# Kernel tuning notes

Measured on AMD Instinct MI355X. Metric: run time of the kernel, lower is better.

The kernel has to match this reference:

```python
import jax, jax.numpy as jnp
import numpy as np

HUMAN_EXHALATION_FLOW = 0.0052  # ENV_CONFIG.HUMAN_EXHALATION_FLOW
TIME_STEP = 1.0                 # ENV_CONFIG.TIME_STEP
N_NODES = 100_000
N_EDGES = 3_200_000
IN_DIM, OUT_DIM, K = 4, 1, 3
T_HIST = 16


def setup_inputs() -> dict:
    key = jax.random.key(0)
    k1, k2, k3, k4, k5 = jax.random.split(key, 5)
    # columns at [:, -1, :]: 0=concentration, 1=people, 2=size (size divides -> keep away from 0)
    origin_data = jax.random.uniform(k1, (N_NODES, T_HIST, 3), jnp.float32, 0.5, 1.5)
    # raw flow field: conv with kernel K (VALID) maps [E+K-1, K, IN_DIM] -> [E, 1, OUT_DIM]
    flow = jax.random.normal(k2, (N_EDGES + K - 1, K, IN_DIM), jnp.float32)
    edge_index = jax.random.randint(k3, (2, N_EDGES), 0, N_NODES, jnp.int32)
    conv_w = jax.random.normal(k4, (OUT_DIM, IN_DIM, K, K), jnp.float32) * 0.1
    conv_b = jax.random.normal(k5, (OUT_DIM,), jnp.float32) * 0.1
    return {"origin_data": origin_data, "flow": flow, "conv_w": conv_w,
            "conv_b": conv_b, "edge_index": edge_index}


def _flow_conv(flow, conv_w, conv_b):
    # [H, W, C] -> [1, C, H, W] -> conv -> [H', W', out_dim]
    x = jnp.transpose(flow, (2, 0, 1))[None]
    y = jax.lax.conv_general_dilated(
        x, conv_w, window_strides=(1, 1), padding='VALID',
        dimension_numbers=('NCHW', 'OIHW', 'NCHW'))
    y = y + conv_b[None, :, None, None]
    return jnp.transpose(y[0], (1, 2, 0))  # [E, 1, out_dim]


def reference(origin_data, flow, conv_w, conv_b, edge_index):
    concentration = origin_data[:, -1, 0]  # [N]
    people = origin_data[:, -1, 1]         # [N]
    size = origin_data[:, -1, 2]           # [N]
    n = concentration.shape[0]
    mask = jnp.ones((n,), concentration.dtype).at[-1].set(0.0)

    fc = _flow_conv(flow, conv_w, conv_b)  # [E, 1, 1]
    val = fc[:, 0, 0]                      # [E]

    src, dst = edge_index[0], edge_index[1]
    # original loop uses .item() everywhere -> these terms are detached from autodiff
    c_sg = jax.lax.stop_gradient(concentration)
    s_sg = jax.lax.stop_gradient(size)
    v_sg = jax.lax.stop_gradient(val)
    msg = jnp.where(src != dst, v_sg * c_sg[src], 0.0)  # skip self-loops
    node_new = jnp.zeros((n,), concentration.dtype)
    node_new = node_new.at[src].add(-msg / s_sg[src] * TIME_STEP)
    node_new = node_new.at[dst].add(msg / s_sg[dst] * TIME_STEP)

    exhaled = HUMAN_EXHALATION_FLOW * jax.lax.stop_gradient(people) / s_sg  # .item() loop -> detached
    result = concentration + (node_new + exhaled * TIME_STEP) * mask
    out2 = jnp.concatenate([edge_index.T.astype(val.dtype), fc[:, :, 0]], axis=1)  # [E, 3]
    return result[:, None], out2
```

## Files before the change

### kernel.cpp

```cpp
#include <hip/hip_runtime.h>


#define WSH  13
#define WSZ  8192
#define SL   20
#define EPT  4
#define MAXW 32

#define OWSH 13
#define OWSZ 8192
#define OPB  16
#define OFPS 8192.0f
#define OQBIAS (1 << 20)
#define OQCLMP ((1 << 19) - 1)

__global__ __launch_bounds__(256) void prep(
    const float* __restrict__ od,
    float* __restrict__ conc,
    unsigned long long* __restrict__ acc,
    unsigned* __restrict__ tails,
    int n_nodes)
{
    if (blockIdx.x == 0 && tails && threadIdx.x < 65)
        tails[(size_t)threadIdx.x << 4] = 0u;
    int n = blockIdx.x * blockDim.x + threadIdx.x;
    if (n >= n_nodes) return;
    conc[n] = od[(long long)n * 48 + 45];
    if (acc) acc[n] = 0ULL;
}

__global__ __launch_bounds__(256) void edge_scatter(
    const float* __restrict__ flow, const int* __restrict__ ei,
    const float* __restrict__ conv_w, const float* __restrict__ conv_b,
    const float* __restrict__ conc,
    float* __restrict__ out2,
    uint2* __restrict__ recA, uint2* __restrict__ recB,
    uint2* __restrict__ ovf,
    unsigned* __restrict__ tails,
    int n_edges, unsigned cap, unsigned ocap)
{
    __shared__ float w[40];
    __shared__ unsigned cnt[2 * MAXW];
    __shared__ unsigned bas[2 * MAXW];
    const int t = threadIdx.x;
    if (t < 36) {
        int i  = t & 3;
        int kw = (t >> 2) % 3;
        int kh = t / 12;
        w[t] = conv_w[i * 9 + kh * 3 + kw];
    }
    if (t == 36) w[36] = conv_b[0];
    if (t < 2 * MAXW) cnt[t] = 0u;
    __syncthreads();

    const long long eb = (long long)blockIdx.x * (256 * EPT) + t;
    int      sN[EPT], dN[EPT];
    float    vA[EPT], vB[EPT];
    unsigned pA_[EPT], pB_[EPT];
    bool     live[EPT];

#pragma unroll
    for (int k = 0; k < EPT; ++k) {
        long long e = eb + (long long)k * 256;
        live[k] = false;
        if (e < n_edges) {
            int s = ei[e];
            int d = ei[n_edges + e];
            const float4* fp = (const float4*)(flow + e * 12);
            float acc = w[36];
#pragma unroll
            for (int q = 0; q < 9; ++q) {
                float4 v = fp[q];
                acc = fmaf(v.x, w[q * 4 + 0], acc);
                acc = fmaf(v.y, w[q * 4 + 1], acc);
                acc = fmaf(v.z, w[q * 4 + 2], acc);
                acc = fmaf(v.w, w[q * 4 + 3], acc);
            }
            float cs = conc[s];
            float* o = out2 + e * 3;
            o[0] = (float)s;
            o[1] = (float)d;
            o[2] = acc;
            sN[k] = s; dN[k] = d;
            vA[k] = acc; vB[k] = acc * cs;
            if (s != d) {
                live[k] = true;
                pA_[k] = atomicAdd(&cnt[(unsigned)s >> WSH], 1u);
                pB_[k] = atomicAdd(&cnt[MAXW + ((unsigned)d >> WSH)], 1u);
            }
        }
    }
    __syncthreads();
    if (t < 2 * MAXW && cnt[t])
        bas[t] = atomicAdd(&tails[(size_t)t << 4], cnt[t]);
    __syncthreads();

#pragma unroll
    for (int k = 0; k < EPT; ++k) {
        if (!live[k]) continue;
        {
            unsigned wa = (unsigned)sN[k] >> WSH;
            unsigned sa = bas[wa] + pA_[k];
            uint2 r; r.x = (unsigned)sN[k]; r.y = __float_as_uint(vA[k]);
            if (sa < cap) {
                recA[(size_t)wa * cap + sa] = r;
            } else {
                unsigned os = atomicAdd(&tails[(size_t)64 << 4], 1u);
                if (os < ocap) ovf[os] = r;
            }
        }
        {
            unsigned wb = (unsigned)dN[k] >> WSH;
            unsigned sb = bas[MAXW + wb] + pB_[k];
            uint2 r; r.x = (unsigned)dN[k]; r.y = __float_as_uint(vB[k]);
            if (sb < cap) {
                recB[(size_t)wb * cap + sb] = r;
            } else {
                r.x |= 0x80000000u;
                unsigned os = atomicAdd(&tails[(size_t)64 << 4], 1u);
                if (os < ocap) ovf[os] = r;
            }
        }
    }
}

__global__ __launch_bounds__(1024) void accum_b(
    const uint2* __restrict__ recA, const uint2* __restrict__ recB,
    const uint2* __restrict__ ovf,
    const unsigned* __restrict__ tails,
    float* __restrict__ pA, float* __restrict__ pB,
    unsigned cap, unsigned ocap)
{
    __shared__ float tA[WSZ];
    __shared__ float tB[WSZ];

    const int w  = blockIdx.x / SL;
    const int sl = blockIdx.x % SL;
    const int t  = threadIdx.x;

    for (int i = t; i < WSZ; i += 1024) { tA[i] = 0.f; tB[i] = 0.f; }
    __syncthreads();

    {
        unsigned nA = min(tails[(size_t)w << 4], cap);
        const uint2* r = recA + (size_t)w * cap;
        size_t i0 = (size_t)nA * sl / SL, i1 = (size_t)nA * (sl + 1) / SL;
        for (size_t i = i0 + t; i < i1; i += 1024) {
            uint2 q = r[i];
            atomicAdd(&tA[q.x & (WSZ - 1)], __uint_as_float(q.y));
        }
    }
    {
        unsigned nB = min(tails[(size_t)(MAXW + w) << 4], cap);
        const uint2* r = recB + (size_t)w * cap;
        size_t i0 = (size_t)nB * sl / SL, i1 = (size_t)nB * (sl + 1) / SL;
        for (size_t i = i0 + t; i < i1; i += 1024) {
            uint2 q = r[i];
            atomicAdd(&tB[q.x & (WSZ - 1)], __uint_as_float(q.y));
        }
    }
    {
        unsigned no = min(tails[(size_t)64 << 4], ocap);
        if (no) {
            size_t i0 = (size_t)no * sl / SL, i1 = (size_t)no * (sl + 1) / SL;
            for (size_t i = i0 + t; i < i1; i += 1024) {
                uint2 q = ovf[i];
                unsigned node = q.x & 0x7fffffffu;
                if ((int)(node >> WSH) == w) {
                    if (q.x >> 31) atomicAdd(&tB[node & (WSZ - 1)], __uint_as_float(q.y));
                    else           atomicAdd(&tA[node & (WSZ - 1)], __uint_as_float(q.y));
                }
            }
        }
    }
    __syncthreads();

    float* dA = pA + ((size_t)blockIdx.x << WSH);
    float* dB = pB + ((size_t)blockIdx.x << WSH);
    for (int i = t; i < (WSZ >> 2); i += 1024) {
        ((float4*)dA)[i] = ((const float4*)tA)[i];
        ((float4*)dB)[i] = ((const float4*)tB)[i];
    }
}

__global__ __launch_bounds__(256) void node_final_b(
    const float* __restrict__ od,
    const float* __restrict__ conc,
    const float* __restrict__ pA,
    const float* __restrict__ pB,
    float* __restrict__ out, int n_nodes)
{
    int n = blockIdx.x * blockDim.x + threadIdx.x;
    if (n >= n_nodes) return;

    const int w = n >> WSH, i = n & (WSZ - 1);
    size_t base = ((size_t)(w * SL) << WSH) + i;
    float a = 0.f, b = 0.f;
#pragma unroll
    for (int sl = 0; sl < SL; ++sl) {
        a += pA[base + ((size_t)sl << WSH)];
        b += pB[base + ((size_t)sl << WSH)];
    }

    long long bi = (long long)n * 48 + 45;
    float c  = conc[n];
    float p  = od[bi + 1];
    float is = 1.0f / od[bi + 2];

    float r = c;
    if (n != n_nodes - 1)
        r += (b - a * c) * is + 0.0052f * p * is;
    out[n] = r;
}

__global__ __launch_bounds__(256) void edge_conv_o(
    const float* __restrict__ flow, const int* __restrict__ ei,
    const float* __restrict__ conv_w, const float* __restrict__ conv_b,
    float* __restrict__ out2, int n_edges)
{
    __shared__ float w[40];
    int t = threadIdx.x;
    if (t < 36) {
        int i  = t & 3;
        int kw = (t >> 2) % 3;
        int kh = t / 12;
        w[t] = conv_w[i * 9 + kh * 3 + kw];
    }
    if (t == 36) w[36] = conv_b[0];
    __syncthreads();

    int e = blockIdx.x * blockDim.x + t;
    if (e >= n_edges) return;

    const float4* fp = (const float4*)(flow + (long long)e * 12);
    float acc = w[36];
#pragma unroll
    for (int q = 0; q < 9; ++q) {
        float4 v = fp[q];
        acc = fmaf(v.x, w[q * 4 + 0], acc);
        acc = fmaf(v.y, w[q * 4 + 1], acc);
        acc = fmaf(v.z, w[q * 4 + 2], acc);
        acc = fmaf(v.w, w[q * 4 + 3], acc);
    }

    float* o = out2 + (long long)e * 3;
    o[0] = (float)ei[e];
    o[1] = (float)ei[n_edges + e];
    o[2] = acc;
}

__global__ __launch_bounds__(1024) void accum_o(
    const float* __restrict__ out2,
    const float* __restrict__ conc,
    unsigned long long* __restrict__ acc,
    int n_edges, int n_nodes)
{
    __shared__ float tA[OWSZ];
    __shared__ float tB[OWSZ];

    const int w    = blockIdx.x / OPB;
    const int sl   = blockIdx.x % OPB;
    const int base = w << OWSH;

    for (int i = threadIdx.x; i < OWSZ; i += 1024) { tA[i] = 0.f; tB[i] = 0.f; }
    __syncthreads();

    const long long e0 = (long long)sl * n_edges / OPB;
    const long long e1 = (long long)(sl + 1) * n_edges / OPB;
    for (long long e = e0 + threadIdx.x; e < e1; e += 1024) {
        const float* r = out2 + e * 3;
        float fs = r[0], fd = r[1], v = r[2];
        int s = (int)fs, d = (int)fd;
        if (s == d) continue;
        if ((s >> OWSH) == w) atomicAdd(&tA[s - base], v);
        if ((d >> OWSH) == w) atomicAdd(&tB[d - base], v * conc[s]);
    }
    __syncthreads();

    for (int i = threadIdx.x; i < OWSZ; i += 1024) {
        int n = base + i;
        if (n >= n_nodes) continue;
        float a = tA[i], b = tB[i];
        if (a == 0.f && b == 0.f) continue;
        int qa = __float2int_rn(a * OFPS);
        int qb = __float2int_rn(b * OFPS);
        qa = min(max(qa, -OQCLMP), OQCLMP);
        qb = min(max(qb, -OQCLMP), OQCLMP);
        unsigned long long enc =
            ((unsigned long long)(unsigned)(qa + OQBIAS) << 37) +
            ((unsigned long long)(unsigned)(qb + OQBIAS) << 10) + 1ULL;
        atomicAdd(acc + n, enc);
    }
}

__global__ __launch_bounds__(256) void node_final_o(
    const float* __restrict__ od,
    const float* __restrict__ conc,
    const unsigned long long* __restrict__ acc,
    float* __restrict__ out, int n_nodes)
{
    int n = blockIdx.x * blockDim.x + threadIdx.x;
    if (n >= n_nodes) return;

    unsigned long long t = acc[n];
    long long cnt = (long long)(t & 1023ULL);
    unsigned long long t2 = t >> 10;
    long long sbr = (long long)(t2 & ((1ULL << 27) - 1));
    long long sar = (long long)(t2 >> 27);
    float a = (float)(sar - cnt * OQBIAS) * (1.0f / OFPS);
    float b = (float)(sbr - cnt * OQBIAS) * (1.0f / OFPS);

    long long bi = (long long)n * 48 + 45;
    float c  = conc[n];
    float p  = od[bi + 1];
    float is = 1.0f / od[bi + 2];

    float r = c;
    if (n != n_nodes - 1)
        r += (b - a * c) * is + 0.0052f * p * is;
    out[n] = r;
}

extern "C" void kernel_launch(void* const* d_in, const int* in_sizes, int n_in,
                              void* d_out, int out_size, void* d_ws, size_t ws_size,
                              hipStream_t stream) {
    const float* od   = (const float*)d_in[0];
    const float* flow = (const float*)d_in[1];
    const float* cw   = (const float*)d_in[2];
    const float* cb   = (const float*)d_in[3];
    const int*   ei   = (const int*)d_in[4];

    const int n_nodes = in_sizes[0] / 48;
    const int n_edges = in_sizes[4] / 2;

    float* out_res = (float*)d_out;
    float* out2    = out_res + n_nodes;

    dim3 blk(256);
    dim3 grid_nodes((n_nodes + 255) / 256);

    const int n_win = (n_nodes + WSZ - 1) >> WSH;
    const unsigned cap  = (unsigned)(n_edges / (n_win > 0 ? n_win : 1))
                        + (unsigned)(n_edges / 8) + 1024u;
    const unsigned ocap = (unsigned)(2ULL * (unsigned long long)n_edges);

    size_t off = 0;
    size_t o_conc  = off; off += (((size_t)n_nodes * 4) + 255) & ~255ULL;
    size_t o_tails = off; off += (65 * 16 * 4 + 255) & ~255ULL;
    size_t o_recA  = off; off += (((size_t)n_win * cap * 8) + 255) & ~255ULL;
    size_t o_recB  = off; off += (((size_t)n_win * cap * 8) + 255) & ~255ULL;
    size_t o_ovf   = off; off += (((size_t)ocap * 8) + 255) & ~255ULL;
    size_t o_pA    = off; off += (((size_t)n_win * SL * WSZ * 4) + 255) & ~255ULL;
    size_t o_pB    = off; off += (((size_t)n_win * SL * WSZ * 4) + 255) & ~255ULL;
    const bool full = (ws_size >= off) && (n_win <= MAXW);

    float* conc = (float*)((char*)d_ws + o_conc);

    if (full) {
        unsigned* tails = (unsigned*)((char*)d_ws + o_tails);
        uint2* recA = (uint2*)((char*)d_ws + o_recA);
        uint2* recB = (uint2*)((char*)d_ws + o_recB);
        uint2* ovf  = (uint2*)((char*)d_ws + o_ovf);
        float* pA   = (float*)((char*)d_ws + o_pA);
        float* pB   = (float*)((char*)d_ws + o_pB);

        dim3 grid_es((n_edges + 256 * EPT - 1) / (256 * EPT));

        prep<<<grid_nodes, blk, 0, stream>>>(od, conc, nullptr, tails, n_nodes);
        edge_scatter<<<grid_es, blk, 0, stream>>>(flow, ei, cw, cb, conc,
                                                  out2, recA, recB, ovf, tails,
                                                  n_edges, cap, ocap);
        accum_b<<<dim3(n_win * SL), dim3(1024), 0, stream>>>(
            recA, recB, ovf, tails, pA, pB, cap, ocap);
        node_final_b<<<grid_nodes, blk, 0, stream>>>(od, conc, pA, pB,
                                                     out_res, n_nodes);
    } else {
        unsigned long long* acc =
            (unsigned long long*)((char*)d_ws + (((size_t)n_nodes * 4 + 7) / 8 * 8));
        const int n_win_o = (n_nodes + OWSZ - 1) >> OWSH;
        dim3 grid_edges((n_edges + 255) / 256);

        prep<<<grid_nodes, blk, 0, stream>>>(od, conc, acc, nullptr, n_nodes);
        edge_conv_o<<<grid_edges, blk, 0, stream>>>(flow, ei, cw, cb, out2, n_edges);
        accum_o<<<dim3(n_win_o * OPB), dim3(1024), 0, stream>>>(
            out2, conc, acc, n_edges, n_nodes);
        node_final_o<<<grid_nodes, blk, 0, stream>>>(od, conc, acc,
                                                     out_res, n_nodes);
    }
}
```

Measured before the change: 341.4 us.

## Stage scatter records in LDS, coalesce writes, and use wider node windows

The edge scatter kernel now sorts each block's records by bucket in shared memory and writes them out contiguously, so the global record stores are coalesced instead of scattered. Window size doubles to 16K nodes with 32 slices per window, which reduces the number of buckets and changes the accumulation grid. The recA/recB buffers merge into one bucketed array, and the partial-sum reduction is split into two accumulators. The cost is extra LDS use (about 24KB per block) and an added barrier in edge_scatter, plus larger per-block shared tables in accum_b, which may lower occupancy.

Measured after the change: 344.1 us. Within noise of the previous version (+0.8%).

```diff
diff --git a/kernel.cpp b/kernel.cpp
--- a/kernel.cpp
+++ b/kernel.cpp
@@ -1,11 +1,12 @@
 #include <hip/hip_runtime.h>
 
 
-#define WSH  13
-#define WSZ  8192
-#define SL   20
-#define EPT  4
-#define MAXW 32
+#define WSH    14
+#define WSZ    16384
+#define SLC    32
+#define EPT    4
+#define MAXWIN 16
+#define OVSLOT 32
 
 #define OWSH 13
 #define OWSZ 8192
@@ -21,7 +22,7 @@
     unsigned* __restrict__ tails,
     int n_nodes)
 {
-    if (blockIdx.x == 0 && tails && threadIdx.x < 65)
+    if (blockIdx.x == 0 && tails && threadIdx.x <= OVSLOT)
         tails[(size_t)threadIdx.x << 4] = 0u;
     int n = blockIdx.x * blockDim.x + threadIdx.x;
     if (n >= n_nodes) return;
@@ -34,15 +35,21 @@
     const float* __restrict__ conv_w, const float* __restrict__ conv_b,
     const float* __restrict__ conc,
     float* __restrict__ out2,
-    uint2* __restrict__ recA, uint2* __restrict__ recB,
+    uint2* __restrict__ rec,
     uint2* __restrict__ ovf,
     unsigned* __restrict__ tails,
-    int n_edges, unsigned cap, unsigned ocap)
-{
-    __shared__ float w[40];
-    __shared__ unsigned cnt[2 * MAXW];
-    __shared__ unsigned bas[2 * MAXW];
-    const int t = threadIdx.x;
+    int n_edges, int n_win, unsigned cap, unsigned ocap)
+{
+    __shared__ float    w[40];
+    __shared__ unsigned cnt[2 * MAXWIN];
+    __shared__ unsigned sst[2 * MAXWIN];
+    __shared__ unsigned bas[2 * MAXWIN];
+    __shared__ unsigned stot;
+    __shared__ uint2    stg[512 * EPT];
+    __shared__ unsigned dsti[512 * EPT];
+
+    const int t  = threadIdx.x;
+    const int NB = 2 * n_win;
     if (t < 36) {
         int i  = t & 3;
         int kw = (t >> 2) % 3;
@@ -50,19 +57,17 @@
         w[t] = conv_w[i * 9 + kh * 3 + kw];
     }
     if (t == 36) w[36] = conv_b[0];
-    if (t < 2 * MAXW) cnt[t] = 0u;
+    if (t < 2 * MAXWIN) cnt[t] = 0u;
     __syncthreads();
 
     const long long eb = (long long)blockIdx.x * (256 * EPT) + t;
-    int      sN[EPT], dN[EPT];
-    float    vA[EPT], vB[EPT];
-    unsigned pA_[EPT], pB_[EPT];
-    bool     live[EPT];
+    uint2    payA[EPT], payB[EPT];
+    unsigned posA[EPT], posB[EPT];
 
 #pragma unroll
     for (int k = 0; k < EPT; ++k) {
+        posA[k] = 0xffffffffu; posB[k] = 0xffffffffu;
         long long e = eb + (long long)k * 256;
-        live[k] = false;
         if (e < n_edges) {
             int s = ei[e];
             int d = ei[n_edges + e];
@@ -81,89 +86,107 @@
             o[0] = (float)s;
             o[1] = (float)d;
             o[2] = acc;
-            sN[k] = s; dN[k] = d;
-            vA[k] = acc; vB[k] = acc * cs;
             if (s != d) {
-                live[k] = true;
-                pA_[k] = atomicAdd(&cnt[(unsigned)s >> WSH], 1u);
-                pB_[k] = atomicAdd(&cnt[MAXW + ((unsigned)d >> WSH)], 1u);
+                payA[k].x = (unsigned)s; payA[k].y = __float_as_uint(acc);
+                payB[k].x = (unsigned)d; payB[k].y = __float_as_uint(acc * cs);
+                posA[k] = atomicAdd(&cnt[(unsigned)s >> WSH], 1u);
+                posB[k] = atomicAdd(&cnt[n_win + ((unsigned)d >> WSH)], 1u);
             }
         }
     }
     __syncthreads();
-    if (t < 2 * MAXW && cnt[t])
-        bas[t] = atomicAdd(&tails[(size_t)t << 4], cnt[t]);
+
+    if (t == 0) {
+        unsigned a = 0;
+        for (int b = 0; b < NB; ++b) { sst[b] = a; a += cnt[b]; }
+        stot = a;
+    }
+    if (t < NB && cnt[t]) bas[t] = atomicAdd(&tails[(size_t)t << 4], cnt[t]);
     __syncthreads();
 
 #pragma unroll
     for (int k = 0; k < EPT; ++k) {
-        if (!live[k]) continue;
-        {
-            unsigned wa = (unsigned)sN[k] >> WSH;
-            unsigned sa = bas[wa] + pA_[k];
-            uint2 r; r.x = (unsigned)sN[k]; r.y = __float_as_uint(vA[k]);
-            if (sa < cap) {
-                recA[(size_t)wa * cap + sa] = r;
+        if (posA[k] != 0xffffffffu) {
+            unsigned b = payA[k].x >> WSH;
+            unsigned i = sst[b] + posA[k];
+            unsigned g = bas[b] + posA[k];
+            stg[i] = payA[k];
+            if (g < cap) {
+                dsti[i] = b * cap + g;
             } else {
-                unsigned os = atomicAdd(&tails[(size_t)64 << 4], 1u);
-                if (os < ocap) ovf[os] = r;
+                dsti[i] = 0xffffffffu;
+                unsigned os = atomicAdd(&tails[(size_t)OVSLOT << 4], 1u);
+                if (os < ocap) ovf[os] = payA[k];
             }
         }
-        {
-            unsigned wb = (unsigned)dN[k] >> WSH;
-            unsigned sb = bas[MAXW + wb] + pB_[k];
-            uint2 r; r.x = (unsigned)dN[k]; r.y = __float_as_uint(vB[k]);
-            if (sb < cap) {
-                recB[(size_t)wb * cap + sb] = r;
+        if (posB[k] != 0xffffffffu) {
+            unsigned b = n_win + (payB[k].x >> WSH);
+            unsigned i = sst[b] + posB[k];
+            unsigned g = bas[b] + posB[k];
+            stg[i] = payB[k];
+            if (g < cap) {
+                dsti[i] = b * cap + g;
             } else {
-                r.x |= 0x80000000u;
-                unsigned os = atomicAdd(&tails[(size_t)64 << 4], 1u);
-                if (os < ocap) ovf[os] = r;
+                dsti[i] = 0xffffffffu;
+                unsigned os = atomicAdd(&tails[(size_t)OVSLOT << 4], 1u);
+                if (os < ocap) { uint2 r = payB[k]; r.x |= 0x80000000u; ovf[os] = r; }
             }
         }
     }
+    __syncthreads();
+
+    unsigned tot = stot;
+    for (unsigned i = t; i < tot; i += 256) {
+        unsigned u = dsti[i];
+        if (u != 0xffffffffu) rec[u] = stg[i];
+    }
 }
 
 __global__ __launch_bounds__(1024) void accum_b(
-    const uint2* __restrict__ recA, const uint2* __restrict__ recB,
-    const uint2* __restrict__ ovf,
+    const uint2* __restrict__ rec, const uint2* __restrict__ ovf,
     const unsigned* __restrict__ tails,
     float* __restrict__ pA, float* __restrict__ pB,
-    unsigned cap, unsigned ocap)
+    int n_win, unsigned cap, unsigned ocap)
 {
     __shared__ float tA[WSZ];
     __shared__ float tB[WSZ];
 
-    const int w  = blockIdx.x / SL;
-    const int sl = blockIdx.x % SL;
+    const int w  = blockIdx.x / SLC;
+    const int sl = blockIdx.x % SLC;
     const int t  = threadIdx.x;
 
-    for (int i = t; i < WSZ; i += 1024) { tA[i] = 0.f; tB[i] = 0.f; }
+    float4 z = make_float4(0.f, 0.f, 0.f, 0.f);
+    for (int i = t; i < (WSZ >> 2); i += 1024) {
+        ((float4*)tA)[i] = z; ((float4*)tB)[i] = z;
+    }
     __syncthreads();
 
     {
         unsigned nA = min(tails[(size_t)w << 4], cap);
-        const uint2* r = recA + (size_t)w * cap;
-        size_t i0 = (size_t)nA * sl / SL, i1 = (size_t)nA * (sl + 1) / SL;
-        for (size_t i = i0 + t; i < i1; i += 1024) {
+        const uint2* r = rec + (size_t)w * cap;
+        unsigned i0 = (unsigned)((unsigned long long)nA * sl / SLC);
+        unsigned i1 = (unsigned)((unsigned long long)nA * (sl + 1) / SLC);
+        for (unsigned i = i0 + t; i < i1; i += 1024) {
             uint2 q = r[i];
             atomicAdd(&tA[q.x & (WSZ - 1)], __uint_as_float(q.y));
         }
     }
     {
-        unsigned nB = min(tails[(size_t)(MAXW + w) << 4], cap);
-        const uint2* r = recB + (size_t)w * cap;
-        size_t i0 = (size_t)nB * sl / SL, i1 = (size_t)nB * (sl + 1) / SL;
-        for (size_t i = i0 + t; i < i1; i += 1024) {
+        unsigned nB = min(tails[(size_t)(n_win + w) << 4], cap);
+        const uint2* r = rec + (size_t)(n_win + w) * cap;
+        unsigned i0 = (unsigned)((unsigned long long)nB * sl / SLC);
+        unsigned i1 = (unsigned)((unsigned long long)nB * (sl + 1) / SLC);
+        for (unsigned i = i0 + t; i < i1; i += 1024) {
             uint2 q = r[i];
             atomicAdd(&tB[q.x & (WSZ - 1)], __uint_as_float(q.y));
         }
     }
     {
-        unsigned no = min(tails[(size_t)64 << 4], ocap);
+        unsigned no = min(tails[(size_t)OVSLOT << 4], ocap);
         if (no) {
-            size_t i0 = (size_t)no * sl / SL, i1 = (size_t)no * (sl + 1) / SL;
-            for (size_t i = i0 + t; i < i1; i += 1024) {
+            unsigned i0 = (unsigned)((unsigned long long)no * sl / SLC);
+            unsigned i1 = (unsigned)((unsigned long long)no * (sl + 1) / SLC);
+            for (unsigned i = i0 + t; i < i1; i += 1024) {
                 uint2 q = ovf[i];
                 unsigned node = q.x & 0x7fffffffu;
                 if ((int)(node >> WSH) == w) {
@@ -194,13 +217,16 @@
     if (n >= n_nodes) return;
 
     const int w = n >> WSH, i = n & (WSZ - 1);
-    size_t base = ((size_t)(w * SL) << WSH) + i;
-    float a = 0.f, b = 0.f;
+    size_t base = ((size_t)(w * SLC) << WSH) + i;
+    float a0 = 0.f, a1 = 0.f, b0 = 0.f, b1 = 0.f;
 #pragma unroll
-    for (int sl = 0; sl < SL; ++sl) {
-        a += pA[base + ((size_t)sl << WSH)];
-        b += pB[base + ((size_t)sl << WSH)];
-    }
+    for (int sl = 0; sl < SLC; sl += 2) {
+        a0 += pA[base + ((size_t)(sl + 0) << WSH)];
+        a1 += pA[base + ((size_t)(sl + 1) << WSH)];
+        b0 += pB[base + ((size_t)(sl + 0) << WSH)];
+        b1 += pB[base + ((size_t)(sl + 1) << WSH)];
+    }
+    float a = a0 + a1, b = b0 + b1;
 
     long long bi = (long long)n * 48 + 45;
     float c  = conc[n];
@@ -340,38 +366,37 @@
     dim3 grid_nodes((n_nodes + 255) / 256);
 
     const int n_win = (n_nodes + WSZ - 1) >> WSH;
+    const int NB    = 2 * n_win;
     const unsigned cap  = (unsigned)(n_edges / (n_win > 0 ? n_win : 1))
-                        + (unsigned)(n_edges / 8) + 1024u;
+                        + (unsigned)(n_edges / 8) + 4096u;
     const unsigned ocap = (unsigned)(2ULL * (unsigned long long)n_edges);
 
     size_t off = 0;
     size_t o_conc  = off; off += (((size_t)n_nodes * 4) + 255) & ~255ULL;
-    size_t o_tails = off; off += (65 * 16 * 4 + 255) & ~255ULL;
-    size_t o_recA  = off; off += (((size_t)n_win * cap * 8) + 255) & ~255ULL;
-    size_t o_recB  = off; off += (((size_t)n_win * cap * 8) + 255) & ~255ULL;
+    size_t o_tails = off; off += ((OVSLOT + 1) * 16 * 4 + 255) & ~255ULL;
+    size_t o_rec   = off; off += (((size_t)NB * cap * 8) + 255) & ~255ULL;
     size_t o_ovf   = off; off += (((size_t)ocap * 8) + 255) & ~255ULL;
-    size_t o_pA    = off; off += (((size_t)n_win * SL * WSZ * 4) + 255) & ~255ULL;
-    size_t o_pB    = off; off += (((size_t)n_win * SL * WSZ * 4) + 255) & ~255ULL;
-    const bool full = (ws_size >= off) && (n_win <= MAXW);
+    size_t o_pA    = off; off += (((size_t)n_win * SLC * WSZ * 4) + 255) & ~255ULL;
+    size_t o_pB    = off; off += (((size_t)n_win * SLC * WSZ * 4) + 255) & ~255ULL;
+    const bool full = (ws_size >= off) && (n_win <= MAXWIN);
 
     float* conc = (float*)((char*)d_ws + o_conc);
 
     if (full) {
         unsigned* tails = (unsigned*)((char*)d_ws + o_tails);
-        uint2* recA = (uint2*)((char*)d_ws + o_recA);
-        uint2* recB = (uint2*)((char*)d_ws + o_recB);
-        uint2* ovf  = (uint2*)((char*)d_ws + o_ovf);
-        float* pA   = (float*)((char*)d_ws + o_pA);
-        float* pB   = (float*)((char*)d_ws + o_pB);
+        uint2* rec = (uint2*)((char*)d_ws + o_rec);
+        uint2* ovf = (uint2*)((char*)d_ws + o_ovf);
+        float* pA  = (float*)((char*)d_ws + o_pA);
+        float* pB  = (float*)((char*)d_ws + o_pB);
 
         dim3 grid_es((n_edges + 256 * EPT - 1) / (256 * EPT));
 
         prep<<<grid_nodes, blk, 0, stream>>>(od, conc, nullptr, tails, n_nodes);
         edge_scatter<<<grid_es, blk, 0, stream>>>(flow, ei, cw, cb, conc,
-                                                  out2, recA, recB, ovf, tails,
-                                                  n_edges, cap, ocap);
-        accum_b<<<dim3(n_win * SL), dim3(1024), 0, stream>>>(
-            recA, recB, ovf, tails, pA, pB, cap, ocap);
+                                                  out2, rec, ovf, tails,
+                                                  n_edges, n_win, cap, ocap);
+        accum_b<<<dim3(n_win * SLC), dim3(1024), 0, stream>>>(
+            rec, ovf, tails, pA, pB, n_win, cap, ocap);
         node_final_b<<<grid_nodes, blk, 0, stream>>>(od, conc, pA, pB,
                                                      out_res, n_nodes);
     } else {
```
